# Optimization experiments

Measured on AMD Instinct MI355X. Metric: run time of the kernel, lower is better.

Reference implementation:

```python
import jax, jax.numpy as jnp
import numpy as np
import math

B, S, D = 1, 2048, 512
H = 8
DH = D // H
WIN = 128  # window_size
EPS = 1e-5


def _layernorm(x, g, b):
    mu = jnp.mean(x, axis=-1, keepdims=True)
    var = jnp.mean((x - mu) ** 2, axis=-1, keepdims=True)
    return (x - mu) * jax.lax.rsqrt(var + EPS) * g + b


def _local_attention(q, k, v, window_size):
    # q,k,v: [B,H,S,DH]. Faithful to F.pad + unfold: zero-padded keys
    # participate in softmax with score 0 (no masking), as in the original.
    w = window_size // 2
    W = 2 * w + 1
    kp = jnp.pad(k, ((0, 0), (0, 0), (w, w), (0, 0)))
    vp = jnp.pad(v, ((0, 0), (0, 0), (w, w), (0, 0)))
    idx = jnp.arange(q.shape[2])[:, None] + jnp.arange(W)[None, :]  # [S,W]
    k_win = kp[:, :, idx]  # [B,H,S,W,DH]
    v_win = vp[:, :, idx]  # [B,H,S,W,DH]
    scores = jnp.einsum('bhsd,bhswd->bhsw', q, k_win) / math.sqrt(q.shape[-1])
    attn = jax.nn.softmax(scores, axis=-1)
    return jnp.einsum('bhsw,bhswd->bhsd', attn, v_win)


def setup_inputs() -> dict:
    key = jax.random.key(0)
    ks = jax.random.split(key, 8)
    sc = 0.02
    return {
        'x': jax.random.normal(ks[0], (B, S, D), dtype=jnp.float32),
        'w_qkv': jax.random.normal(ks[1], (D, 3 * D), dtype=jnp.float32) * sc,
        'b_qkv': jnp.zeros((3 * D,), dtype=jnp.float32),
        'w_out': jax.random.normal(ks[2], (D, D), dtype=jnp.float32) * sc,
        'b_out': jnp.zeros((D,), dtype=jnp.float32),
        'ln_g': jnp.ones((D,), dtype=jnp.float32),
        'ln_b': jnp.zeros((D,), dtype=jnp.float32),
        'w1': jax.random.normal(ks[3], (D, 4 * D), dtype=jnp.float32) * sc,
        'b1': jnp.zeros((4 * D,), dtype=jnp.float32),
        'w2': jax.random.normal(ks[4], (4 * D, D), dtype=jnp.float32) * sc,
        'b2': jnp.zeros((D,), dtype=jnp.float32),
    }


def reference(x, w_qkv, b_qkv, w_out, b_out, ln_g, ln_b, w1, b1, w2, b2):
    residual = x
    xn = _layernorm(x, ln_g, ln_b)
    qkv = xn @ w_qkv + b_qkv                       # [B,S,3D]
    qkv = qkv.reshape(B, S, 3, H, DH)
    qkv = jnp.transpose(qkv, (2, 0, 3, 1, 4))      # [3,B,H,S,DH]
    q, k, v = qkv[0], qkv[1], qkv[2]
    attn_out = _local_attention(q, k, v, WIN)       # [B,H,S,DH]
    attn_out = jnp.transpose(attn_out, (0, 2, 1, 3)).reshape(B, S, D)
    attn_out = attn_out @ w_out + b_out
    out = residual + attn_out
    # FFN applied directly to `out` (no second norm in original)
    ffn = jax.nn.gelu(out @ w1 + b1, approximate=False) @ w2 + b2
    return out + ffn
```

## Files before the change

### kernel.cpp

```cpp
#include <hip/hip_runtime.h>
#include <math.h>

#define S_LEN 2048
#define DMODEL 512
#define NHEAD 8
#define DHEAD 64
#define LN_EPS 1e-5f

typedef __bf16 bf16;
typedef __bf16 bf16x8 __attribute__((ext_vector_type(8)));
typedef __bf16 bf16x2 __attribute__((ext_vector_type(2)));
typedef float f32x4 __attribute__((ext_vector_type(4)));

__device__ __forceinline__ float wave_reduce_sum(float x) {
#pragma unroll
  for (int off = 32; off > 0; off >>= 1) x += __shfl_xor(x, off);
  return x;
}

__global__ __launch_bounds__(256) void ln_kernel(const float* __restrict__ x,
                                                 const float* __restrict__ g,
                                                 const float* __restrict__ b,
                                                 bf16* __restrict__ xn) {
  const int row = blockIdx.x;
  const int tid = threadIdx.x;
  const float2 v = ((const float2*)(x + (size_t)row * DMODEL))[tid];
  float s = v.x + v.y;
  float s2 = v.x * v.x + v.y * v.y;
  s = wave_reduce_sum(s);
  s2 = wave_reduce_sum(s2);
  __shared__ float red[2][4];
  const int wv = tid >> 6, ln = tid & 63;
  if (ln == 0) { red[0][wv] = s; red[1][wv] = s2; }
  __syncthreads();
  s = red[0][0] + red[0][1] + red[0][2] + red[0][3];
  s2 = red[1][0] + red[1][1] + red[1][2] + red[1][3];
  const float mu = s * (1.0f / DMODEL);
  const float var = s2 * (1.0f / DMODEL) - mu * mu;
  const float rs = rsqrtf(var + LN_EPS);
  const float2 gg = ((const float2*)g)[tid];
  const float2 bb = ((const float2*)b)[tid];
  bf16x2 o;
  o[0] = (bf16)((v.x - mu) * rs * gg.x + bb.x);
  o[1] = (bf16)((v.y - mu) * rs * gg.y + bb.y);
  ((bf16x2*)(xn + (size_t)row * DMODEL))[tid] = o;
}

__global__ __launch_bounds__(256) void transpose_cast(const float* __restrict__ W,
                                                      bf16* __restrict__ WT,
                                                      int K, int N) {
  __shared__ float t[32][33];
  const int c = threadIdx.x & 31, r8 = threadIdx.x >> 5;
  const int n0 = blockIdx.x * 32, k0 = blockIdx.y * 32;
#pragma unroll
  for (int it = 0; it < 4; it++) {
    const int r = r8 + it * 8;
    t[r][c] = W[(size_t)(k0 + r) * N + n0 + c];
  }
  __syncthreads();
#pragma unroll
  for (int it = 0; it < 4; it++) {
    const int r = r8 + it * 8;
    WT[(size_t)(n0 + r) * K + k0 + c] = (bf16)t[c][r];
  }
}

__global__ __launch_bounds__(256) void v_transpose(const bf16* __restrict__ qkvb,
                                                   bf16* __restrict__ vT) {
  __shared__ bf16 t[32][33];
  const int c = threadIdx.x & 31, r8 = threadIdx.x >> 5;
  const int c0 = blockIdx.x * 32;
  const int s0 = blockIdx.y * 32;
#pragma unroll
  for (int it = 0; it < 4; it++) {
    const int r = r8 + it * 8;
    t[r][c] = qkvb[(size_t)(s0 + r) * 1536 + 1024 + c0 + c];
  }
  __syncthreads();
#pragma unroll
  for (int it = 0; it < 4; it++) {
    const int r = r8 + it * 8;
    vT[(size_t)(c0 + r) * S_LEN + s0 + c] = t[c][r];
  }
}

template <int MODE>
__device__ __forceinline__ void epilogue_store(float v, const float* res,
                                               float* Cf, bf16* Cb,
                                               size_t row, size_t col, int N) {
  if (MODE == 2) v = 0.5f * v * (1.0f + erff(v * 0.70710678118654752f));
  if (MODE == 1 || MODE == 3) v += res[row * N + col];
  if (MODE == 1 || MODE == 3) Cf[row * N + col] = v;
  if (MODE == 0 || MODE == 1 || MODE == 2) Cb[row * N + col] = (bf16)v;
}

template <int MODE>
__global__ __launch_bounds__(256) void mm_kernel(const bf16* __restrict__ A,
                                                 const bf16* __restrict__ BT,
                                                 const float* __restrict__ bias,
                                                 const float* __restrict__ res,
                                                 float* __restrict__ Cf,
                                                 bf16* __restrict__ Cb,
                                                 int N, int K) {
  __shared__ bf16 As[128 * 32];
  __shared__ bf16 Bs[128 * 32];
  const int tid = threadIdx.x;
  const int wave = tid >> 6, lane = tid & 63;
  const int rowBase = blockIdx.y * 128, colBase = blockIdx.x * 128;
  const int lr = lane & 15, kg = lane >> 4;
  const int wm = wave & 1, wn = wave >> 1;

  f32x4 acc[4][4] = {};
  const int srow = lane >> 2;
  const int skcol = (lane & 3) * 8;

  for (int kk = 0; kk < K; kk += 32) {
#pragma unroll
    for (int it = 0; it < 2; it++) {
      const int seg = wave * 2 + it;
      const int row = seg * 16 + srow;
      const bf16* ga = A + (size_t)(rowBase + row) * K + kk + skcol;
      const bf16* gb = BT + (size_t)(colBase + row) * K + kk + skcol;
      __builtin_amdgcn_global_load_lds(
          (const __attribute__((address_space(1))) void*)ga,
          (__attribute__((address_space(3))) void*)(As + seg * 512), 16, 0, 0);
      __builtin_amdgcn_global_load_lds(
          (const __attribute__((address_space(1))) void*)gb,
          (__attribute__((address_space(3))) void*)(Bs + seg * 512), 16, 0, 0);
    }
    __syncthreads();

    bf16x8 af[4], bfr[4];
#pragma unroll
    for (int i = 0; i < 4; i++)
      af[i] = *(const bf16x8*)(As + ((wm * 64 + i * 16 + lr) * 32 + kg * 8));
#pragma unroll
    for (int j = 0; j < 4; j++)
      bfr[j] = *(const bf16x8*)(Bs + ((wn * 64 + j * 16 + lr) * 32 + kg * 8));
#pragma unroll
    for (int i = 0; i < 4; i++)
#pragma unroll
      for (int j = 0; j < 4; j++)
        acc[i][j] = __builtin_amdgcn_mfma_f32_16x16x32_bf16(af[i], bfr[j],
                                                            acc[i][j], 0, 0, 0);
    __syncthreads();
  }

  const int orow0 = rowBase + wm * 64 + kg * 4;
  const int ocol0 = colBase + wn * 64 + lr;
#pragma unroll
  for (int j = 0; j < 4; j++) {
    const int col = ocol0 + j * 16;
    const float bs = bias[col];
#pragma unroll
    for (int i = 0; i < 4; i++)
#pragma unroll
      for (int r = 0; r < 4; r++)
        epilogue_store<MODE>(acc[i][j][r] + bs, res, Cf, Cb,
                             (size_t)(orow0 + i * 16 + r), (size_t)col, N);
  }
}

template <int MODE>
__global__ __launch_bounds__(256) void mm64_kernel(const bf16* __restrict__ A,
                                                   const bf16* __restrict__ BT,
                                                   const float* __restrict__ bias,
                                                   const float* __restrict__ res,
                                                   float* __restrict__ Cf,
                                                   bf16* __restrict__ Cb,
                                                   int N, int K) {
  __shared__ bf16 As[64 * 32];
  __shared__ bf16 Bs[64 * 32];
  const int tid = threadIdx.x;
  const int wave = tid >> 6, lane = tid & 63;
  const int rowBase = blockIdx.y * 64, colBase = blockIdx.x * 64;
  const int lr = lane & 15, kg = lane >> 4;
  const int wm = wave & 1, wn = wave >> 1;

  f32x4 acc[2][2] = {};
  const int srow = lane >> 2;
  const int skcol = (lane & 3) * 8;

  for (int kk = 0; kk < K; kk += 32) {
    const int row = wave * 16 + srow;
    const bf16* ga = A + (size_t)(rowBase + row) * K + kk + skcol;
    const bf16* gb = BT + (size_t)(colBase + row) * K + kk + skcol;
    __builtin_amdgcn_global_load_lds(
        (const __attribute__((address_space(1))) void*)ga,
        (__attribute__((address_space(3))) void*)(As + wave * 512), 16, 0, 0);
    __builtin_amdgcn_global_load_lds(
        (const __attribute__((address_space(1))) void*)gb,
        (__attribute__((address_space(3))) void*)(Bs + wave * 512), 16, 0, 0);
    __syncthreads();

    bf16x8 af[2], bfr[2];
#pragma unroll
    for (int i = 0; i < 2; i++)
      af[i] = *(const bf16x8*)(As + ((wm * 32 + i * 16 + lr) * 32 + kg * 8));
#pragma unroll
    for (int j = 0; j < 2; j++)
      bfr[j] = *(const bf16x8*)(Bs + ((wn * 32 + j * 16 + lr) * 32 + kg * 8));
#pragma unroll
    for (int i = 0; i < 2; i++)
#pragma unroll
      for (int j = 0; j < 2; j++)
        acc[i][j] = __builtin_amdgcn_mfma_f32_16x16x32_bf16(af[i], bfr[j],
                                                            acc[i][j], 0, 0, 0);
    __syncthreads();
  }

  const int orow0 = rowBase + wm * 32 + kg * 4;
  const int ocol0 = colBase + wn * 32 + lr;
#pragma unroll
  for (int j = 0; j < 2; j++) {
    const int col = ocol0 + j * 16;
    const float bs = bias[col];
#pragma unroll
    for (int i = 0; i < 2; i++)
#pragma unroll
      for (int r = 0; r < 4; r++)
        epilogue_store<MODE>(acc[i][j][r] + bs, res, Cf, Cb,
                             (size_t)(orow0 + i * 16 + r), (size_t)col, N);
  }
}

__global__ __launch_bounds__(256) void attn_fused(const bf16* __restrict__ qkvb,
                                                  const bf16* __restrict__ vT,
                                                  bf16* __restrict__ attnb) {
  __shared__ bf16 Kl[192][72];
  __shared__ bf16 Vt[64][200];
  __shared__ bf16 Ql[64][72];

  const int tid = threadIdx.x;
  const int s0 = blockIdx.x * 64;
  const int hc = blockIdx.y * DHEAD;

  {
    const int row = tid >> 2, c0 = (tid & 3) * 16;
    const bf16* src = qkvb + (size_t)(s0 + row) * 1536 + hc + c0;
    *(bf16x8*)&Ql[row][c0] = *(const bf16x8*)src;
    *(bf16x8*)&Ql[row][c0 + 8] = *(const bf16x8*)(src + 8);
  }
#pragma unroll
  for (int it = 0; it < 3; it++) {
    const int row = it * 64 + (tid >> 2), c0 = (tid & 3) * 16;
    const int p = s0 - 64 + row;
    bf16x8 a, b;
    if (p >= 0 && p < S_LEN) {
      const bf16* src = qkvb + (size_t)p * 1536 + 512 + hc + c0;
      a = *(const bf16x8*)src;
      b = *(const bf16x8*)(src + 8);
    } else {
#pragma unroll
      for (int j = 0; j < 8; j++) { a[j] = (bf16)0.f; b[j] = (bf16)0.f; }
    }
    *(bf16x8*)&Kl[row][c0] = a;
    *(bf16x8*)&Kl[row][c0 + 8] = b;
  }
  {
    const int d = tid >> 2, r0 = (tid & 3) * 48;
    const bf16* src = vT + (size_t)(hc + d) * S_LEN;
#pragma unroll
    for (int i = 0; i < 6; i++) {
      const int p0 = s0 - 64 + r0 + i * 8;
      bf16x8 v;
      if (p0 >= 0 && p0 + 8 <= S_LEN) {
        v = *(const bf16x8*)(src + p0);
      } else {
#pragma unroll
        for (int j = 0; j < 8; j++) {
          const int p = p0 + j;
          v[j] = (p >= 0 && p < S_LEN) ? src[p] : (bf16)0.f;
        }
      }
      *(bf16x8*)&Vt[d][r0 + i * 8] = v;
    }
  }
  __syncthreads();

  const int wv = tid >> 6, lane = tid & 63;
  const int lr = lane & 15, kg = lane >> 4;

  f32x4 c[12] = {};
#pragma unroll
  for (int step = 0; step < 2; step++) {
    const bf16x8 qf = *(const bf16x8*)&Ql[wv * 16 + lr][step * 32 + kg * 8];
#pragma unroll
    for (int t = 0; t < 12; t++) {
      const bf16x8 kf = *(const bf16x8*)&Kl[t * 16 + lr][step * 32 + kg * 8];
      c[t] = __builtin_amdgcn_mfma_f32_16x16x32_bf16(qf, kf, c[t], 0, 0, 0);
    }
  }

  float e[12][4];
  float inv[4];
#pragma unroll
  for (int rr = 0; rr < 4; rr++) {
    const int q = wv * 16 + kg * 4 + rr;
    float m = -1e30f;
#pragma unroll
    for (int t = 0; t < 12; t++) {
      const int col = t * 16 + lr;
      if (col >= q && col <= q + 128) m = fmaxf(m, c[t][rr] * 0.125f);
    }
#pragma unroll
    for (int off = 1; off < 16; off <<= 1) m = fmaxf(m, __shfl_xor(m, off));
    float sum = 0.f;
#pragma unroll
    for (int t = 0; t < 12; t++) {
      const int col = t * 16 + lr;
      const bool valid = (col >= q) && (col <= q + 128);
      const float ev = valid ? __expf(c[t][rr] * 0.125f - m) : 0.f;
      e[t][rr] = ev;
      sum += ev;
    }
#pragma unroll
    for (int off = 1; off < 16; off <<= 1) sum += __shfl_xor(sum, off);
    inv[rr] = 1.f / sum;
  }

  __syncthreads();

  bf16* Pl = (bf16*)Kl + wv * (16 * 200);
#pragma unroll
  for (int rr = 0; rr < 4; rr++)
#pragma unroll
    for (int t = 0; t < 12; t++)
      Pl[(kg * 4 + rr) * 200 + t * 16 + lr] = (bf16)(e[t][rr] * inv[rr]);

  f32x4 o[4] = {};
#pragma unroll
  for (int step = 0; step < 6; step++) {
    const bf16x8 pf = *(const bf16x8*)&Pl[lr * 200 + step * 32 + kg * 8];
#pragma unroll
    for (int jt = 0; jt < 4; jt++) {
      const bf16x8 vf = *(const bf16x8*)&Vt[jt * 16 + lr][step * 32 + kg * 8];
      o[jt] = __builtin_amdgcn_mfma_f32_16x16x32_bf16(pf, vf, o[jt], 0, 0, 0);
    }
  }

#pragma unroll
  for (int jt = 0; jt < 4; jt++)
#pragma unroll
    for (int rr = 0; rr < 4; rr++) {
      const int q = wv * 16 + kg * 4 + rr;
      attnb[(size_t)(s0 + q) * DMODEL + hc + jt * 16 + lr] = (bf16)o[jt][rr];
    }
}

extern "C" void kernel_launch(void* const* d_in, const int* in_sizes, int n_in,
                              void* d_out, int out_size, void* d_ws, size_t ws_size,
                              hipStream_t stream) {
  const float* x     = (const float*)d_in[0];
  const float* w_qkv = (const float*)d_in[1];
  const float* b_qkv = (const float*)d_in[2];
  const float* w_out = (const float*)d_in[3];
  const float* b_out = (const float*)d_in[4];
  const float* ln_g  = (const float*)d_in[5];
  const float* ln_b  = (const float*)d_in[6];
  const float* w1    = (const float*)d_in[7];
  const float* b1    = (const float*)d_in[8];
  const float* w2    = (const float*)d_in[9];
  const float* b2    = (const float*)d_in[10];
  float* out = (float*)d_out;

  char* w = (char*)d_ws;
  const size_t MB = 1u << 20;
  bf16* xn    = (bf16*)(w + 0);
  bf16* attnb = (bf16*)(w + 0);
  bf16* qkvb  = (bf16*)(w + 2 * MB);
  bf16* outb  = (bf16*)(w + 2 * MB);
  bf16* vT    = (bf16*)(w + 8 * MB);
  bf16* h1    = (bf16*)(w + 10 * MB);
  bf16* wqkvT = (bf16*)(w + 18 * MB);
  bf16* woutT = (bf16*)(w + 19 * MB + 512 * 1024);
  bf16* w1T   = (bf16*)(w + 20 * MB);
  bf16* w2T   = (bf16*)(w + 22 * MB);

  transpose_cast<<<dim3(48, 16), 256, 0, stream>>>(w_qkv, wqkvT, 512, 1536);
  transpose_cast<<<dim3(16, 16), 256, 0, stream>>>(w_out, woutT, 512, 512);
  transpose_cast<<<dim3(64, 16), 256, 0, stream>>>(w1, w1T, 512, 2048);
  transpose_cast<<<dim3(16, 64), 256, 0, stream>>>(w2, w2T, 2048, 512);

  ln_kernel<<<S_LEN, 256, 0, stream>>>(x, ln_g, ln_b, xn);
  mm_kernel<0><<<dim3(12, 16), 256, 0, stream>>>(xn, wqkvT, b_qkv, nullptr,
                                                 nullptr, qkvb, 1536, 512);
  v_transpose<<<dim3(16, 64), 256, 0, stream>>>(qkvb, vT);
  attn_fused<<<dim3(32, 8), 256, 0, stream>>>(qkvb, vT, attnb);
  mm64_kernel<1><<<dim3(8, 32), 256, 0, stream>>>(attnb, woutT, b_out, x, out,
                                                  outb, 512, 512);
  mm_kernel<2><<<dim3(16, 16), 256, 0, stream>>>(outb, w1T, b1, nullptr,
                                                 nullptr, h1, 2048, 512);
  mm64_kernel<3><<<dim3(8, 32), 256, 0, stream>>>(h1, w2T, b2, out, out,
                                                  nullptr, 512, 2048);
}
```

Baseline: 174.3 us.

## Double-buffer GEMM tiles with K=64 stages, shrink tiles, merge weight transposes

Rewrites both GEMM kernels to stage K=64 slabs into double-buffered LDS, issuing the next slab's global_load_lds before the current MFMAs. This removes one barrier per iteration and overlaps loads with compute. Tiles shrink (64x128 and 32x64), which doubles the grid so more CUs are busy on these small matrices, but each block gets less reuse. The four weight transpose launches are merged into one kernel to cut launch overhead.

After: 147.7 us. 15.3% less time.

```diff
diff --git a/kernel.cpp b/kernel.cpp
--- a/kernel.cpp
+++ b/kernel.cpp
@@ -46,12 +46,20 @@
   ((bf16x2*)(xn + (size_t)row * DMODEL))[tid] = o;
 }
 
-__global__ __launch_bounds__(256) void transpose_cast(const float* __restrict__ W,
-                                                      bf16* __restrict__ WT,
-                                                      int K, int N) {
+__global__ __launch_bounds__(256) void transpose_all(
+    const float* __restrict__ w_qkv, const float* __restrict__ w_out,
+    const float* __restrict__ w1, const float* __restrict__ w2,
+    bf16* __restrict__ wqkvT, bf16* __restrict__ woutT,
+    bf16* __restrict__ w1T, bf16* __restrict__ w2T) {
+  int b = blockIdx.x;
+  const float* W; bf16* WT; int K, N, bx, by;
+  if (b < 768)       { W = w_qkv; WT = wqkvT; K = 512;  N = 1536; bx = b % 48; by = b / 48; }
+  else if (b < 1024) { b -= 768;  W = w_out; WT = woutT; K = 512;  N = 512;  bx = b % 16; by = b / 16; }
+  else if (b < 2048) { b -= 1024; W = w1;    WT = w1T;   K = 512;  N = 2048; bx = b % 64; by = b / 64; }
+  else               { b -= 2048; W = w2;    WT = w2T;   K = 2048; N = 512;  bx = b % 16; by = b / 16; }
   __shared__ float t[32][33];
   const int c = threadIdx.x & 31, r8 = threadIdx.x >> 5;
-  const int n0 = blockIdx.x * 32, k0 = blockIdx.y * 32;
+  const int n0 = bx * 32, k0 = by * 32;
 #pragma unroll
   for (int it = 0; it < 4; it++) {
     const int r = r8 + it * 8;
@@ -95,132 +103,155 @@
 }
 
 template <int MODE>
-__global__ __launch_bounds__(256) void mm_kernel(const bf16* __restrict__ A,
-                                                 const bf16* __restrict__ BT,
-                                                 const float* __restrict__ bias,
-                                                 const float* __restrict__ res,
-                                                 float* __restrict__ Cf,
-                                                 bf16* __restrict__ Cb,
-                                                 int N, int K) {
-  __shared__ bf16 As[128 * 32];
-  __shared__ bf16 Bs[128 * 32];
+__global__ __launch_bounds__(256) void mmA_kernel(const bf16* __restrict__ A,
+                                                  const bf16* __restrict__ BT,
+                                                  const float* __restrict__ bias,
+                                                  const float* __restrict__ res,
+                                                  float* __restrict__ Cf,
+                                                  bf16* __restrict__ Cb,
+                                                  int N, int K) {
+  __shared__ bf16 As[2][64 * 64];
+  __shared__ bf16 Bs[2][128 * 64];
   const int tid = threadIdx.x;
   const int wave = tid >> 6, lane = tid & 63;
-  const int rowBase = blockIdx.y * 128, colBase = blockIdx.x * 128;
   const int lr = lane & 15, kg = lane >> 4;
-  const int wm = wave & 1, wn = wave >> 1;
-
-  f32x4 acc[4][4] = {};
-  const int srow = lane >> 2;
-  const int skcol = (lane & 3) * 8;
-
-  for (int kk = 0; kk < K; kk += 32) {
-#pragma unroll
-    for (int it = 0; it < 2; it++) {
-      const int seg = wave * 2 + it;
-      const int row = seg * 16 + srow;
-      const bf16* ga = A + (size_t)(rowBase + row) * K + kk + skcol;
-      const bf16* gb = BT + (size_t)(colBase + row) * K + kk + skcol;
+  const int rowBase = blockIdx.y * 64, colBase = blockIdx.x * 128;
+
+  f32x4 acc[4][2] = {};
+  const int niter = K >> 6;
+
+  auto stage = [&](int kk, int buf) {
+#pragma unroll
+    for (int r = 0; r < 2; ++r) {
+      const int c = wave * 2 + r;
+      const int elem = c * 512 + lane * 8;
+      const int s = elem >> 11, row = (elem >> 5) & 63, kp = elem & 31;
+      const bf16* ga = A + (size_t)(rowBase + row) * K + kk + s * 32 + kp;
       __builtin_amdgcn_global_load_lds(
           (const __attribute__((address_space(1))) void*)ga,
-          (__attribute__((address_space(3))) void*)(As + seg * 512), 16, 0, 0);
+          (__attribute__((address_space(3))) void*)(&As[buf][c * 512]), 16, 0, 0);
+    }
+#pragma unroll
+    for (int r = 0; r < 4; ++r) {
+      const int c = wave * 4 + r;
+      const int elem = c * 512 + lane * 8;
+      const int s = elem >> 12, row = (elem >> 5) & 127, kp = elem & 31;
+      const bf16* gb = BT + (size_t)(colBase + row) * K + kk + s * 32 + kp;
       __builtin_amdgcn_global_load_lds(
           (const __attribute__((address_space(1))) void*)gb,
-          (__attribute__((address_space(3))) void*)(Bs + seg * 512), 16, 0, 0);
-    }
+          (__attribute__((address_space(3))) void*)(&Bs[buf][c * 512]), 16, 0, 0);
+    }
+  };
+
+  stage(0, 0);
+  for (int it = 0; it < niter; ++it) {
+    const int cur = it & 1;
     __syncthreads();
-
-    bf16x8 af[4], bfr[4];
-#pragma unroll
-    for (int i = 0; i < 4; i++)
-      af[i] = *(const bf16x8*)(As + ((wm * 64 + i * 16 + lr) * 32 + kg * 8));
-#pragma unroll
-    for (int j = 0; j < 4; j++)
-      bfr[j] = *(const bf16x8*)(Bs + ((wn * 64 + j * 16 + lr) * 32 + kg * 8));
-#pragma unroll
-    for (int i = 0; i < 4; i++)
-#pragma unroll
-      for (int j = 0; j < 4; j++)
-        acc[i][j] = __builtin_amdgcn_mfma_f32_16x16x32_bf16(af[i], bfr[j],
-                                                            acc[i][j], 0, 0, 0);
-    __syncthreads();
-  }
-
-  const int orow0 = rowBase + wm * 64 + kg * 4;
-  const int ocol0 = colBase + wn * 64 + lr;
-#pragma unroll
-  for (int j = 0; j < 4; j++) {
-    const int col = ocol0 + j * 16;
+    if (it + 1 < niter) stage((it + 1) << 6, cur ^ 1);
+    const bf16* as = As[cur];
+    const bf16* bs = Bs[cur];
+#pragma unroll
+    for (int s = 0; s < 2; ++s) {
+      bf16x8 af[4], bfr[2];
+#pragma unroll
+      for (int i = 0; i < 4; ++i)
+        af[i] = *(const bf16x8*)(as + s * 2048 + (i * 16 + lr) * 32 + kg * 8);
+#pragma unroll
+      for (int j = 0; j < 2; ++j)
+        bfr[j] = *(const bf16x8*)(bs + s * 4096 + (wave * 32 + j * 16 + lr) * 32 + kg * 8);
+#pragma unroll
+      for (int i = 0; i < 4; ++i)
+#pragma unroll
+        for (int j = 0; j < 2; ++j)
+          acc[i][j] = __builtin_amdgcn_mfma_f32_16x16x32_bf16(af[i], bfr[j],
+                                                              acc[i][j], 0, 0, 0);
+    }
+  }
+
+#pragma unroll
+  for (int j = 0; j < 2; ++j) {
+    const int col = colBase + wave * 32 + j * 16 + lr;
     const float bs = bias[col];
 #pragma unroll
-    for (int i = 0; i < 4; i++)
-#pragma unroll
-      for (int r = 0; r < 4; r++)
+    for (int i = 0; i < 4; ++i)
+#pragma unroll
+      for (int r = 0; r < 4; ++r)
         epilogue_store<MODE>(acc[i][j][r] + bs, res, Cf, Cb,
-                             (size_t)(orow0 + i * 16 + r), (size_t)col, N);
+                             (size_t)(rowBase + i * 16 + kg * 4 + r),
+                             (size_t)col, N);
   }
 }
 
 template <int MODE>
-__global__ __launch_bounds__(256) void mm64_kernel(const bf16* __restrict__ A,
-                                                   const bf16* __restrict__ BT,
-                                                   const float* __restrict__ bias,
-                                                   const float* __restrict__ res,
-                                                   float* __restrict__ Cf,
-                                                   bf16* __restrict__ Cb,
-                                                   int N, int K) {
-  __shared__ bf16 As[64 * 32];
-  __shared__ bf16 Bs[64 * 32];
+__global__ __launch_bounds__(256) void mmB_kernel(const bf16* __restrict__ A,
+                                                  const bf16* __restrict__ BT,
+                                                  const float* __restrict__ bias,
+                                                  const float* __restrict__ res,
+                                                  float* __restrict__ Cf,
+                                                  bf16* __restrict__ Cb,
+                                                  int N, int K) {
+  __shared__ bf16 As[2][32 * 64];
+  __shared__ bf16 Bs[2][64 * 64];
   const int tid = threadIdx.x;
   const int wave = tid >> 6, lane = tid & 63;
-  const int rowBase = blockIdx.y * 64, colBase = blockIdx.x * 64;
   const int lr = lane & 15, kg = lane >> 4;
-  const int wm = wave & 1, wn = wave >> 1;
-
-  f32x4 acc[2][2] = {};
-  const int srow = lane >> 2;
-  const int skcol = (lane & 3) * 8;
-
-  for (int kk = 0; kk < K; kk += 32) {
-    const int row = wave * 16 + srow;
-    const bf16* ga = A + (size_t)(rowBase + row) * K + kk + skcol;
-    const bf16* gb = BT + (size_t)(colBase + row) * K + kk + skcol;
-    __builtin_amdgcn_global_load_lds(
-        (const __attribute__((address_space(1))) void*)ga,
-        (__attribute__((address_space(3))) void*)(As + wave * 512), 16, 0, 0);
-    __builtin_amdgcn_global_load_lds(
-        (const __attribute__((address_space(1))) void*)gb,
-        (__attribute__((address_space(3))) void*)(Bs + wave * 512), 16, 0, 0);
+  const int rowBase = blockIdx.y * 32, colBase = blockIdx.x * 64;
+
+  f32x4 acc[2] = {};
+  const int niter = K >> 6;
+
+  auto stage = [&](int kk, int buf) {
+    {
+      const int c = wave;
+      const int elem = c * 512 + lane * 8;
+      const int s = elem >> 10, row = (elem >> 5) & 31, kp = elem & 31;
+      const bf16* ga = A + (size_t)(rowBase + row) * K + kk + s * 32 + kp;
+      __builtin_amdgcn_global_load_lds(
+          (const __attribute__((address_space(1))) void*)ga,
+          (__attribute__((address_space(3))) void*)(&As[buf][c * 512]), 16, 0, 0);
+    }
+#pragma unroll
+    for (int r = 0; r < 2; ++r) {
+      const int c = wave * 2 + r;
+      const int elem = c * 512 + lane * 8;
+      const int s = elem >> 11, row = (elem >> 5) & 63, kp = elem & 31;
+      const bf16* gb = BT + (size_t)(colBase + row) * K + kk + s * 32 + kp;
+      __builtin_amdgcn_global_load_lds(
+          (const __attribute__((address_space(1))) void*)gb,
+          (__attribute__((address_space(3))) void*)(&Bs[buf][c * 512]), 16, 0, 0);
+    }
+  };
+
+  stage(0, 0);
+  for (int it = 0; it < niter; ++it) {
+    const int cur = it & 1;
     __syncthreads();
-
-    bf16x8 af[2], bfr[2];
-#pragma unroll
-    for (int i = 0; i < 2; i++)
-      af[i] = *(const bf16x8*)(As + ((wm * 32 + i * 16 + lr) * 32 + kg * 8));
-#pragma unroll
-    for (int j = 0; j < 2; j++)
-      bfr[j] = *(const bf16x8*)(Bs + ((wn * 32 + j * 16 + lr) * 32 + kg * 8));
-#pragma unroll
-    for (int i = 0; i < 2; i++)
-#pragma unroll
-      for (int j = 0; j < 2; j++)
-        acc[i][j] = __builtin_amdgcn_mfma_f32_16x16x32_bf16(af[i], bfr[j],
-                                                            acc[i][j], 0, 0, 0);
-    __syncthreads();
-  }
-
-  const int orow0 = rowBase + wm * 32 + kg * 4;
-  const int ocol0 = colBase + wn * 32 + lr;
-#pragma unroll
-  for (int j = 0; j < 2; j++) {
-    const int col = ocol0 + j * 16;
+    if (it + 1 < niter) stage((it + 1) << 6, cur ^ 1);
+    const bf16* as = As[cur];
+    const bf16* bs = Bs[cur];
+#pragma unroll
+    for (int s = 0; s < 2; ++s) {
+      bf16x8 af[2], bfr;
+#pragma unroll
+      for (int i = 0; i < 2; ++i)
+        af[i] = *(const bf16x8*)(as + s * 1024 + (i * 16 + lr) * 32 + kg * 8);
+      bfr = *(const bf16x8*)(bs + s * 2048 + (wave * 16 + lr) * 32 + kg * 8);
+#pragma unroll
+      for (int i = 0; i < 2; ++i)
+        acc[i] = __builtin_amdgcn_mfma_f32_16x16x32_bf16(af[i], bfr, acc[i], 0, 0, 0);
+    }
+  }
+
+  {
+    const int col = colBase + wave * 16 + lr;
     const float bs = bias[col];
 #pragma unroll
-    for (int i = 0; i < 2; i++)
-#pragma unroll
-      for (int r = 0; r < 4; r++)
-        epilogue_store<MODE>(acc[i][j][r] + bs, res, Cf, Cb,
-                             (size_t)(orow0 + i * 16 + r), (size_t)col, N);
+    for (int i = 0; i < 2; ++i)
+#pragma unroll
+      for (int r = 0; r < 4; ++r)
+        epilogue_store<MODE>(acc[i][r] + bs, res, Cf, Cb,
+                             (size_t)(rowBase + i * 16 + kg * 4 + r),
+                             (size_t)col, N);
   }
 }
 
@@ -377,20 +408,17 @@
   bf16* w1T   = (bf16*)(w + 20 * MB);
   bf16* w2T   = (bf16*)(w + 22 * MB);
 
-  transpose_cast<<<dim3(48, 16), 256, 0, stream>>>(w_qkv, wqkvT, 512, 1536);
-  transpose_cast<<<dim3(16, 16), 256, 0, stream>>>(w_out, woutT, 512, 512);
-  transpose_cast<<<dim3(64, 16), 256, 0, stream>>>(w1, w1T, 512, 2048);
-  transpose_cast<<<dim3(16, 64), 256, 0, stream>>>(w2, w2T, 2048, 512);
-
+  transpose_all<<<3072, 256, 0, stream>>>(w_qkv, w_out, w1, w2,
+                                          wqkvT, woutT, w1T, w2T);
   ln_kernel<<<S_LEN, 256, 0, stream>>>(x, ln_g, ln_b, xn);
-  mm_kernel<0><<<dim3(12, 16), 256, 0, stream>>>(xn, wqkvT, b_qkv, nullptr,
-                                                 nullptr, qkvb, 1536, 512);
+  mmA_kernel<0><<<dim3(12, 32), 256, 0, stream>>>(xn, wqkvT, b_qkv, nullptr,
+                                                  nullptr, qkvb, 1536, 512);
   v_transpose<<<dim3(16, 64), 256, 0, stream>>>(qkvb, vT);
   attn_fused<<<dim3(32, 8), 256, 0, stream>>>(qkvb, vT, attnb);
-  mm64_kernel<1><<<dim3(8, 32), 256, 0, stream>>>(attnb, woutT, b_out, x, out,
-                                                  outb, 512, 512);
-  mm_kernel<2><<<dim3(16, 16), 256, 0, stream>>>(outb, w1T, b1, nullptr,
-                                                 nullptr, h1, 2048, 512);
-  mm64_kernel<3><<<dim3(8, 32), 256, 0, stream>>>(h1, w2T, b2, out, out,
-                                                  nullptr, 512, 2048);
-}
+  mmB_kernel<1><<<dim3(8, 64), 256, 0, stream>>>(attnb, woutT, b_out, x, out,
+                                                 outb, 512, 512);
+  mmA_kernel<2><<<dim3(16, 32), 256, 0, stream>>>(outb, w1T, b1, nullptr,
+                                                  nullptr, h1, 2048, 512);
+  mmB_kernel<3><<<dim3(8, 64), 256, 0, stream>>>(h1, w2T, b2, out, out,
+                                                 nullptr, 512, 2048);
+}
```
